# Performance work log

Measured on AMD Instinct MI355X. Metric: run time of the kernel, lower is better.

Reference implementation:

```python
import jax, jax.numpy as jnp
import numpy as np

B, F, V, D, ND = 16384, 26, 100000, 64, 13
H1, H2, H3 = 1024, 512, 256


def setup_inputs() -> dict:
    key = jax.random.key(0)
    ks = jax.random.split(key, 12)
    s = 0.02
    return {
        "dense": jax.random.normal(ks[0], (B, ND), jnp.float32),
        "sparse_idx": jax.random.randint(ks[1], (B, F), 0, V),
        "bias": jnp.zeros((1, 1), jnp.float32),
        "emb_tables": jax.random.normal(ks[2], (F, V, D), jnp.float32) * s,
        "lin_tables": jax.random.normal(ks[3], (F, V), jnp.float32) * s,
        "Wd": jax.random.normal(ks[4], (ND, D), jnp.float32) * s,
        "Wld": jax.random.normal(ks[5], (ND, 1), jnp.float32) * s,
        "bld": jnp.zeros((1,), jnp.float32),
        "W1": jax.random.normal(ks[6], ((F + 1) * D, H1), jnp.float32) * s,
        "W2": jax.random.normal(ks[7], (H1, H2), jnp.float32) * s,
        "W3": jax.random.normal(ks[8], (H2, H3), jnp.float32) * s,
        "Wout": jax.random.normal(ks[9], (H3, 1), jnp.float32) * s,
    }


def reference(dense, sparse_idx, bias, emb_tables, lin_tables, Wd, Wld, bld, W1, W2, W3, Wout):
    feat = jnp.arange(F)[None, :]                      # [1,F] broadcasts with idx [B,F]
    sparse_emb = emb_tables[feat, sparse_idx]          # [B,F,D] batched multi-table gather
    dense_emb = dense @ Wd                             # [B,D]
    emb = jnp.concatenate([dense_emb[:, None, :], sparse_emb], axis=1)  # [B,F+1,D]

    # first-order term: linear dense + per-feature 1-dim embeddings
    first = dense @ Wld + bld + lin_tables[feat, sparse_idx].sum(axis=1, keepdims=True)  # [B,1]

    # FM second-order: 0.5 * sum_d ((sum_f e)^2 - sum_f e^2)
    sum_e = emb.sum(axis=1)                            # [B,D]
    second = 0.5 * (sum_e * sum_e - (emb * emb).sum(axis=1)).sum(axis=1, keepdims=True)  # [B,1]

    # deep part (dropout p=0 -> identity)
    h = emb.reshape(emb.shape[0], -1)                  # [B,(F+1)*D]
    h = jax.nn.relu(h @ W1)
    h = jax.nn.relu(h @ W2)
    h = jax.nn.relu(h @ W3)
    deep = h @ Wout                                    # [B,1]

    return bias + first + second + deep
```

## Files before the change

kernel.cpp:

```cpp
#include <hip/hip_runtime.h>
#include <hip/hip_bf16.h>

#define B_SAMP 16384
#define NFEAT 26
#define VOCAB 100000
#define DIM 64
#define NDENSE 13
#define H1 1024
#define H2 512
#define H3 256
#define KIN ((NFEAT + 1) * DIM)

typedef short s16x8 __attribute__((ext_vector_type(8)));
typedef float f32x4 __attribute__((ext_vector_type(4)));

__device__ inline void async_load16(const void* g, void* lds) {
  __builtin_amdgcn_global_load_lds(
      (const __attribute__((address_space(1))) void*)g,
      (__attribute__((address_space(3))) void*)lds, 16, 0, 0);
}

__global__ __launch_bounds__(256) void k_embed_fm(
    const float* __restrict__ dense, const int* __restrict__ sidx,
    const float* __restrict__ emb, const float* __restrict__ lin,
    const float* __restrict__ Wd, const float* __restrict__ Wld,
    const float* __restrict__ bld,
    __hip_bfloat16* __restrict__ h, float* __restrict__ partial)
{
  int wave = threadIdx.x >> 6, lane = threadIdx.x & 63;
  int b = blockIdx.x * 4 + wave;
  const float* drow = dense + b * NDENSE;

  float de = 0.f;
#pragma unroll
  for (int nd = 0; nd < NDENSE; ++nd) de += drow[nd] * Wd[nd * DIM + lane];

  __hip_bfloat16* hrow = h + (size_t)b * KIN;
  hrow[lane] = __float2bfloat16(de);
  float sum_e = de, sumsq = de * de;

  float fo = 0.f;
  if (lane < NDENSE) fo = drow[lane] * Wld[lane];

  const int* irow = sidx + b * NFEAT;
#pragma unroll
  for (int f = 0; f < NFEAT; ++f) {
    int ix = irow[f];
    float e = emb[((size_t)f * VOCAB + ix) * DIM + lane];
    sum_e += e; sumsq += e * e;
    hrow[(f + 1) * DIM + lane] = __float2bfloat16(e);
  }
  if (lane < NFEAT) fo += lin[(size_t)lane * VOCAB + irow[lane]];

  float sec = sum_e * sum_e - sumsq;
#pragma unroll
  for (int o = 32; o > 0; o >>= 1) {
    sec += __shfl_down(sec, o);
    fo  += __shfl_down(fo, o);
  }
  if (lane == 0) partial[b] = fo + bld[0] + 0.5f * sec;
}

__global__ __launch_bounds__(256) void k_transpose_bf16(
    const float* __restrict__ src, __hip_bfloat16* __restrict__ dst, int R, int C)
{
  __shared__ float tile[32][33];
  int c0 = blockIdx.x * 32, r0 = blockIdx.y * 32;
  int tx = threadIdx.x & 31, ty = threadIdx.x >> 5;
#pragma unroll
  for (int i = 0; i < 32; i += 8)
    tile[ty + i][tx] = src[(size_t)(r0 + ty + i) * C + c0 + tx];
  __syncthreads();
#pragma unroll
  for (int i = 0; i < 32; i += 8)
    dst[(size_t)(c0 + ty + i) * R + r0 + tx] = __float2bfloat16(tile[tx][ty + i]);
}

__global__ void k_conv_bf16(const float* __restrict__ src,
                            __hip_bfloat16* __restrict__ dst, int n) {
  int i = blockIdx.x * blockDim.x + threadIdx.x;
  if (i < n) dst[i] = __float2bfloat16(src[i]);
}

template <bool RELU>
__global__ __launch_bounds__(256) void k_gemm_bt(
    const __hip_bfloat16* __restrict__ A,
    const __hip_bfloat16* __restrict__ Bt,
    __hip_bfloat16* __restrict__ C,
    int M, int N, int K)
{
  __shared__ __hip_bfloat16 As[128 * 32];
  __shared__ __hip_bfloat16 Bs[128 * 32];
  int tid = threadIdx.x;
  int wave = tid >> 6, lane = tid & 63;
  int wm = wave & 1, wn = wave >> 1;
  int bm = blockIdx.x * 128, bn = blockIdx.y * 128;
  int quad = lane >> 4, l15 = lane & 15;
  int srow = lane >> 2;
  int schunk = (lane & 3) * 8;

  f32x4 acc[4][4];
#pragma unroll
  for (int i = 0; i < 4; ++i)
#pragma unroll
    for (int j = 0; j < 4; ++j) acc[i][j] = (f32x4){0.f, 0.f, 0.f, 0.f};

  int nk = K >> 5;
  for (int kt = 0; kt < nk; ++kt) {
    int k0 = kt << 5;
    __syncthreads();
#pragma unroll
    for (int i = 0; i < 2; ++i) {
      int row = 64 * i + 16 * wave;
      async_load16(A  + (size_t)(bm + row + srow) * K + k0 + schunk,
                   &As[row * 32]);
      async_load16(Bt + (size_t)(bn + row + srow) * K + k0 + schunk,
                   &Bs[row * 32]);
    }
    __syncthreads();

    s16x8 af[4], bf[4];
#pragma unroll
    for (int i = 0; i < 4; ++i) {
      af[i] = *(const s16x8*)&As[(64 * wm + 16 * i + l15) * 32 + quad * 8];
      bf[i] = *(const s16x8*)&Bs[(64 * wn + 16 * i + l15) * 32 + quad * 8];
    }
#pragma unroll
    for (int mi = 0; mi < 4; ++mi)
#pragma unroll
      for (int ni = 0; ni < 4; ++ni)
        acc[mi][ni] = __builtin_amdgcn_mfma_f32_16x16x32_bf16(
            af[mi], bf[ni], acc[mi][ni], 0, 0, 0);
  }

#pragma unroll
  for (int mi = 0; mi < 4; ++mi)
#pragma unroll
    for (int ni = 0; ni < 4; ++ni)
#pragma unroll
      for (int r = 0; r < 4; ++r) {
        int m = bm + 64 * wm + 16 * mi + quad * 4 + r;
        int n = bn + 64 * wn + 16 * ni + l15;
        float v = acc[mi][ni][r];
        if (RELU) v = fmaxf(v, 0.f);
        C[(size_t)m * N + n] = __float2bfloat16(v);
      }
}

__global__ __launch_bounds__(256) void k_final(
    const __hip_bfloat16* __restrict__ a3, const __hip_bfloat16* __restrict__ wo,
    const float* __restrict__ partial, const float* __restrict__ bias,
    float* __restrict__ out)
{
  int wave = threadIdx.x >> 6, lane = threadIdx.x & 63;
  int b = blockIdx.x * 4 + wave;
  const __hip_bfloat16* row = a3 + (size_t)b * H3;
  float s = 0.f;
#pragma unroll
  for (int i = 0; i < H3 / 64; ++i)
    s += __bfloat162float(row[lane + 64 * i]) * __bfloat162float(wo[lane + 64 * i]);
#pragma unroll
  for (int o = 32; o > 0; o >>= 1) s += __shfl_down(s, o);
  if (lane == 0) out[b] = bias[0] + partial[b] + s;
}

extern "C" void kernel_launch(void* const* d_in, const int* in_sizes, int n_in,
                              void* d_out, int out_size, void* d_ws, size_t ws_size,
                              hipStream_t stream) {
  const float* dense = (const float*)d_in[0];
  const int*   sidx  = (const int*)d_in[1];
  const float* bias  = (const float*)d_in[2];
  const float* emb   = (const float*)d_in[3];
  const float* lin   = (const float*)d_in[4];
  const float* Wd    = (const float*)d_in[5];
  const float* Wld   = (const float*)d_in[6];
  const float* bld   = (const float*)d_in[7];
  const float* W1    = (const float*)d_in[8];
  const float* W2    = (const float*)d_in[9];
  const float* W3    = (const float*)d_in[10];
  const float* Wout  = (const float*)d_in[11];
  float* out = (float*)d_out;

  char* ws = (char*)d_ws;
  const size_t o_h   = 0;
  const size_t o_a2  = 0;
  const size_t o_a3  = 16777216;
  const size_t o_a1  = 56623104;
  const size_t o_w1t = o_a1 + 33554432;
  const size_t o_w2t = o_w1t + 3538944;
  const size_t o_w3t = o_w2t + 1048576;
  const size_t o_wo  = o_w3t + 262144;
  const size_t o_par = o_wo + 512;

  __hip_bfloat16* h   = (__hip_bfloat16*)(ws + o_h);
  __hip_bfloat16* a1  = (__hip_bfloat16*)(ws + o_a1);
  __hip_bfloat16* a2  = (__hip_bfloat16*)(ws + o_a2);
  __hip_bfloat16* a3  = (__hip_bfloat16*)(ws + o_a3);
  __hip_bfloat16* W1t = (__hip_bfloat16*)(ws + o_w1t);
  __hip_bfloat16* W2t = (__hip_bfloat16*)(ws + o_w2t);
  __hip_bfloat16* W3t = (__hip_bfloat16*)(ws + o_w3t);
  __hip_bfloat16* Wob = (__hip_bfloat16*)(ws + o_wo);
  float* partial      = (float*)(ws + o_par);

  k_transpose_bf16<<<dim3(H1 / 32, KIN / 32), 256, 0, stream>>>(W1, W1t, KIN, H1);
  k_transpose_bf16<<<dim3(H2 / 32, H1 / 32), 256, 0, stream>>>(W2, W2t, H1, H2);
  k_transpose_bf16<<<dim3(H3 / 32, H2 / 32), 256, 0, stream>>>(W3, W3t, H2, H3);
  k_conv_bf16<<<1, 256, 0, stream>>>(Wout, Wob, H3);

  k_embed_fm<<<B_SAMP / 4, 256, 0, stream>>>(dense, sidx, emb, lin, Wd, Wld, bld,
                                             h, partial);

  k_gemm_bt<true><<<dim3(B_SAMP / 128, H1 / 128), 256, 0, stream>>>(h,  W1t, a1, B_SAMP, H1, KIN);
  k_gemm_bt<true><<<dim3(B_SAMP / 128, H2 / 128), 256, 0, stream>>>(a1, W2t, a2, B_SAMP, H2, H1);
  k_gemm_bt<true><<<dim3(B_SAMP / 128, H3 / 128), 256, 0, stream>>>(a2, W3t, a3, B_SAMP, H3, H1 / 2);

  k_final<<<B_SAMP / 4, 256, 0, stream>>>(a3, Wob, partial, bias, out);
}
```

Before: 915.8 us.

## Switch MLP GEMMs to FP8 scaled MFMA with padded K layout

Activations and weights are now quantized to FP8 (e4m3) instead of bf16, and the three MLP GEMMs use the 16x16x128 scaled f8f6f4 MFMA with K tiles of 128. The first layer's K is padded from 1728 to 1792 with zeros, and the LDS staging layout is reorganized to match the new fragment shape. The last layer writes fp32 so the final dot product reads Wout in fp32 directly. The aim is more matrix throughput and less memory traffic. The cost is FP8 accuracy: with no per-tensor scaling, values around 0.02 scale lose precision and small activations may underflow, which risks tolerance failures.

```diff
diff --git a/kernel.cpp b/kernel.cpp
--- a/kernel.cpp
+++ b/kernel.cpp
@@ -10,14 +10,20 @@
 #define H2 512
 #define H3 256
 #define KIN ((NFEAT + 1) * DIM)
-
-typedef short s16x8 __attribute__((ext_vector_type(8)));
+#define KP1 1792
+
+typedef int   i32x4 __attribute__((ext_vector_type(4)));
+typedef int   i32x8 __attribute__((ext_vector_type(8)));
 typedef float f32x4 __attribute__((ext_vector_type(4)));
 
 __device__ inline void async_load16(const void* g, void* lds) {
   __builtin_amdgcn_global_load_lds(
       (const __attribute__((address_space(1))) void*)g,
       (__attribute__((address_space(3))) void*)lds, 16, 0, 0);
+}
+
+__device__ inline unsigned char f32_to_fp8(float v) {
+  return (unsigned char)(__builtin_amdgcn_cvt_pk_fp8_f32(v, v, 0, false) & 0xff);
 }
 
 __global__ __launch_bounds__(256) void k_embed_fm(
@@ -25,7 +31,7 @@
     const float* __restrict__ emb, const float* __restrict__ lin,
     const float* __restrict__ Wd, const float* __restrict__ Wld,
     const float* __restrict__ bld,
-    __hip_bfloat16* __restrict__ h, float* __restrict__ partial)
+    unsigned char* __restrict__ h, float* __restrict__ partial)
 {
   int wave = threadIdx.x >> 6, lane = threadIdx.x & 63;
   int b = blockIdx.x * 4 + wave;
@@ -35,8 +41,9 @@
 #pragma unroll
   for (int nd = 0; nd < NDENSE; ++nd) de += drow[nd] * Wd[nd * DIM + lane];
 
-  __hip_bfloat16* hrow = h + (size_t)b * KIN;
-  hrow[lane] = __float2bfloat16(de);
+  unsigned char* hrow = h + (size_t)b * KP1;
+  hrow[lane] = f32_to_fp8(de);
+  hrow[KIN + lane] = 0;
   float sum_e = de, sumsq = de * de;
 
   float fo = 0.f;
@@ -48,7 +55,7 @@
     int ix = irow[f];
     float e = emb[((size_t)f * VOCAB + ix) * DIM + lane];
     sum_e += e; sumsq += e * e;
-    hrow[(f + 1) * DIM + lane] = __float2bfloat16(e);
+    hrow[(f + 1) * DIM + lane] = f32_to_fp8(e);
   }
   if (lane < NFEAT) fo += lin[(size_t)lane * VOCAB + irow[lane]];
 
@@ -61,43 +68,37 @@
   if (lane == 0) partial[b] = fo + bld[0] + 0.5f * sec;
 }
 
-__global__ __launch_bounds__(256) void k_transpose_bf16(
-    const float* __restrict__ src, __hip_bfloat16* __restrict__ dst, int R, int C)
+__global__ __launch_bounds__(256) void k_transpose_fp8(
+    const float* __restrict__ src, unsigned char* __restrict__ dst,
+    int R, int C, int Rp)
 {
   __shared__ float tile[32][33];
   int c0 = blockIdx.x * 32, r0 = blockIdx.y * 32;
   int tx = threadIdx.x & 31, ty = threadIdx.x >> 5;
 #pragma unroll
+  for (int i = 0; i < 32; i += 8) {
+    int r = r0 + ty + i;
+    tile[ty + i][tx] = (r < R) ? src[(size_t)r * C + c0 + tx] : 0.f;
+  }
+  __syncthreads();
+#pragma unroll
   for (int i = 0; i < 32; i += 8)
-    tile[ty + i][tx] = src[(size_t)(r0 + ty + i) * C + c0 + tx];
-  __syncthreads();
-#pragma unroll
-  for (int i = 0; i < 32; i += 8)
-    dst[(size_t)(c0 + ty + i) * R + r0 + tx] = __float2bfloat16(tile[tx][ty + i]);
-}
-
-__global__ void k_conv_bf16(const float* __restrict__ src,
-                            __hip_bfloat16* __restrict__ dst, int n) {
-  int i = blockIdx.x * blockDim.x + threadIdx.x;
-  if (i < n) dst[i] = __float2bfloat16(src[i]);
-}
-
-template <bool RELU>
-__global__ __launch_bounds__(256) void k_gemm_bt(
-    const __hip_bfloat16* __restrict__ A,
-    const __hip_bfloat16* __restrict__ Bt,
-    __hip_bfloat16* __restrict__ C,
-    int M, int N, int K)
-{
-  __shared__ __hip_bfloat16 As[128 * 32];
-  __shared__ __hip_bfloat16 Bs[128 * 32];
+    dst[(size_t)(c0 + ty + i) * Rp + r0 + tx] = f32_to_fp8(tile[tx][ty + i]);
+}
+
+template <bool RELU, bool FP8OUT>
+__global__ __launch_bounds__(256) void k_gemm_fp8(
+    const unsigned char* __restrict__ A,
+    const unsigned char* __restrict__ Bt,
+    void* __restrict__ Cv, int M, int N, int K)
+{
+  __shared__ unsigned char As[16384];
+  __shared__ unsigned char Bs[16384];
   int tid = threadIdx.x;
   int wave = tid >> 6, lane = tid & 63;
   int wm = wave & 1, wn = wave >> 1;
   int bm = blockIdx.x * 128, bn = blockIdx.y * 128;
-  int quad = lane >> 4, l15 = lane & 15;
-  int srow = lane >> 2;
-  int schunk = (lane & 3) * 8;
+  int l15 = lane & 15, quad = lane >> 4;
 
   f32x4 acc[4][4];
 #pragma unroll
@@ -105,32 +106,44 @@
 #pragma unroll
     for (int j = 0; j < 4; ++j) acc[i][j] = (f32x4){0.f, 0.f, 0.f, 0.f};
 
-  int nk = K >> 5;
+  int nk = K >> 7;
   for (int kt = 0; kt < nk; ++kt) {
-    int k0 = kt << 5;
+    int k0 = kt << 7;
     __syncthreads();
 #pragma unroll
-    for (int i = 0; i < 2; ++i) {
-      int row = 64 * i + 16 * wave;
-      async_load16(A  + (size_t)(bm + row + srow) * K + k0 + schunk,
-                   &As[row * 32]);
-      async_load16(Bt + (size_t)(bn + row + srow) * K + k0 + schunk,
-                   &Bs[row * 32]);
+    for (int s = 0; s < 2; ++s) {
+      int st = 2 * wave + s;
+      size_t ga = (size_t)(bm + st * 16 + l15) * K + k0 + quad * 32;
+      size_t gb = (size_t)(bn + st * 16 + l15) * K + k0 + quad * 32;
+#pragma unroll
+      for (int j = 0; j < 2; ++j) {
+        async_load16(A + ga + j * 16, &As[st * 2048 + j * 1024]);
+        async_load16(Bt + gb + j * 16, &Bs[st * 2048 + j * 1024]);
+      }
     }
     __syncthreads();
 
-    s16x8 af[4], bf[4];
+    i32x8 af[4], bf[4];
 #pragma unroll
     for (int i = 0; i < 4; ++i) {
-      af[i] = *(const s16x8*)&As[(64 * wm + 16 * i + l15) * 32 + quad * 8];
-      bf[i] = *(const s16x8*)&Bs[(64 * wn + 16 * i + l15) * 32 + quad * 8];
+      {
+        i32x4 lo = *(const i32x4*)&As[(4 * wm + i) * 2048 + lane * 16];
+        i32x4 hi = *(const i32x4*)&As[(4 * wm + i) * 2048 + 1024 + lane * 16];
+        af[i] = (i32x8){lo.x, lo.y, lo.z, lo.w, hi.x, hi.y, hi.z, hi.w};
+      }
+      {
+        i32x4 lo = *(const i32x4*)&Bs[(4 * wn + i) * 2048 + lane * 16];
+        i32x4 hi = *(const i32x4*)&Bs[(4 * wn + i) * 2048 + 1024 + lane * 16];
+        bf[i] = (i32x8){lo.x, lo.y, lo.z, lo.w, hi.x, hi.y, hi.z, hi.w};
+      }
     }
 #pragma unroll
     for (int mi = 0; mi < 4; ++mi)
 #pragma unroll
       for (int ni = 0; ni < 4; ++ni)
-        acc[mi][ni] = __builtin_amdgcn_mfma_f32_16x16x32_bf16(
-            af[mi], bf[ni], acc[mi][ni], 0, 0, 0);
+        acc[mi][ni] = __builtin_amdgcn_mfma_scale_f32_16x16x128_f8f6f4(
+            af[mi], bf[ni], acc[mi][ni],
+            0 , 0 , 0, 0x7f7f7f7f, 0, 0x7f7f7f7f);
   }
 
 #pragma unroll
@@ -143,22 +156,23 @@
         int n = bn + 64 * wn + 16 * ni + l15;
         float v = acc[mi][ni][r];
         if (RELU) v = fmaxf(v, 0.f);
-        C[(size_t)m * N + n] = __float2bfloat16(v);
+        if (FP8OUT) ((unsigned char*)Cv)[(size_t)m * N + n] = f32_to_fp8(v);
+        else        ((float*)Cv)[(size_t)m * N + n] = v;
       }
 }
 
 __global__ __launch_bounds__(256) void k_final(
-    const __hip_bfloat16* __restrict__ a3, const __hip_bfloat16* __restrict__ wo,
+    const float* __restrict__ a3, const float* __restrict__ wo,
     const float* __restrict__ partial, const float* __restrict__ bias,
     float* __restrict__ out)
 {
   int wave = threadIdx.x >> 6, lane = threadIdx.x & 63;
   int b = blockIdx.x * 4 + wave;
-  const __hip_bfloat16* row = a3 + (size_t)b * H3;
+  const float* row = a3 + (size_t)b * H3;
   float s = 0.f;
 #pragma unroll
   for (int i = 0; i < H3 / 64; ++i)
-    s += __bfloat162float(row[lane + 64 * i]) * __bfloat162float(wo[lane + 64 * i]);
+    s += row[lane + 64 * i] * wo[lane + 64 * i];
 #pragma unroll
   for (int o = 32; o > 0; o >>= 1) s += __shfl_down(s, o);
   if (lane == 0) out[b] = bias[0] + partial[b] + s;
@@ -183,36 +197,33 @@
 
   char* ws = (char*)d_ws;
   const size_t o_h   = 0;
-  const size_t o_a2  = 0;
-  const size_t o_a3  = 16777216;
-  const size_t o_a1  = 56623104;
-  const size_t o_w1t = o_a1 + 33554432;
-  const size_t o_w2t = o_w1t + 3538944;
-  const size_t o_w3t = o_w2t + 1048576;
-  const size_t o_wo  = o_w3t + 262144;
-  const size_t o_par = o_wo + 512;
-
-  __hip_bfloat16* h   = (__hip_bfloat16*)(ws + o_h);
-  __hip_bfloat16* a1  = (__hip_bfloat16*)(ws + o_a1);
-  __hip_bfloat16* a2  = (__hip_bfloat16*)(ws + o_a2);
-  __hip_bfloat16* a3  = (__hip_bfloat16*)(ws + o_a3);
-  __hip_bfloat16* W1t = (__hip_bfloat16*)(ws + o_w1t);
-  __hip_bfloat16* W2t = (__hip_bfloat16*)(ws + o_w2t);
-  __hip_bfloat16* W3t = (__hip_bfloat16*)(ws + o_w3t);
-  __hip_bfloat16* Wob = (__hip_bfloat16*)(ws + o_wo);
-  float* partial      = (float*)(ws + o_par);
-
-  k_transpose_bf16<<<dim3(H1 / 32, KIN / 32), 256, 0, stream>>>(W1, W1t, KIN, H1);
-  k_transpose_bf16<<<dim3(H2 / 32, H1 / 32), 256, 0, stream>>>(W2, W2t, H1, H2);
-  k_transpose_bf16<<<dim3(H3 / 32, H2 / 32), 256, 0, stream>>>(W3, W3t, H2, H3);
-  k_conv_bf16<<<1, 256, 0, stream>>>(Wout, Wob, H3);
+  const size_t o_a1  = 29360128;
+  const size_t o_a2  = 46137344;
+  const size_t o_a3  = 54525952;
+  const size_t o_w1t = 71303168;
+  const size_t o_w2t = 73138176;
+  const size_t o_w3t = 73662464;
+  const size_t o_par = 73793536;
+
+  unsigned char* h   = (unsigned char*)(ws + o_h);
+  unsigned char* a1  = (unsigned char*)(ws + o_a1);
+  unsigned char* a2  = (unsigned char*)(ws + o_a2);
+  float*         a3  = (float*)(ws + o_a3);
+  unsigned char* W1t = (unsigned char*)(ws + o_w1t);
+  unsigned char* W2t = (unsigned char*)(ws + o_w2t);
+  unsigned char* W3t = (unsigned char*)(ws + o_w3t);
+  float* partial     = (float*)(ws + o_par);
+
+  k_transpose_fp8<<<dim3(H1 / 32, KP1 / 32), 256, 0, stream>>>(W1, W1t, KIN, H1, KP1);
+  k_transpose_fp8<<<dim3(H2 / 32, H1 / 32), 256, 0, stream>>>(W2, W2t, H1, H2, H1);
+  k_transpose_fp8<<<dim3(H3 / 32, H2 / 32), 256, 0, stream>>>(W3, W3t, H2, H3, H2);
 
   k_embed_fm<<<B_SAMP / 4, 256, 0, stream>>>(dense, sidx, emb, lin, Wd, Wld, bld,
                                              h, partial);
 
-  k_gemm_bt<true><<<dim3(B_SAMP / 128, H1 / 128), 256, 0, stream>>>(h,  W1t, a1, B_SAMP, H1, KIN);
-  k_gemm_bt<true><<<dim3(B_SAMP / 128, H2 / 128), 256, 0, stream>>>(a1, W2t, a2, B_SAMP, H2, H1);
-  k_gemm_bt<true><<<dim3(B_SAMP / 128, H3 / 128), 256, 0, stream>>>(a2, W3t, a3, B_SAMP, H3, H1 / 2);
-
-  k_final<<<B_SAMP / 4, 256, 0, stream>>>(a3, Wob, partial, bias, out);
-}
+  k_gemm_fp8<true, true ><<<dim3(B_SAMP / 128, H1 / 128), 256, 0, stream>>>(h,  W1t, a1, B_SAMP, H1, KP1);
+  k_gemm_fp8<true, true ><<<dim3(B_SAMP / 128, H2 / 128), 256, 0, stream>>>(a1, W2t, a2, B_SAMP, H2, H1);
+  k_gemm_fp8<true, false><<<dim3(B_SAMP / 128, H3 / 128), 256, 0, stream>>>(a2, W3t, a3, B_SAMP, H3, H2);
+
+  k_final<<<B_SAMP / 4, 256, 0, stream>>>(a3, Wout, partial, bias, out);
+}
```

Result: faster. 861.0 us (-6.0%).
